# Kernel tuning notes

Hardware: AMD Instinct MI355X
Metric: run time of the kernel (lower is better)

The kernel has to match this reference:

```python
import jax, jax.numpy as jnp
import numpy as np

N_NODES = 50000
N_EDGES = 800000
D_FEAT = 256      # node feature dim F
D_HID = 512       # MLP hidden; MLP input is 2*F = 512
D_OUT = 256


def setup_inputs() -> dict:
    key = jax.random.key(0)
    k = jax.random.split(key, 6)
    x = jax.random.normal(k[0], (N_NODES, D_FEAT), dtype=jnp.float32)
    edge_index = jax.random.randint(k[1], (2, N_EDGES), 0, N_NODES, dtype=jnp.int64)
    # Glorot-ish scaled params for the MLP h_Theta: Linear(2F->H) -> ReLU -> Linear(H->O)
    W1 = jax.random.normal(k[2], (2 * D_FEAT, D_HID), dtype=jnp.float32) / np.sqrt(2 * D_FEAT)
    b1 = jnp.zeros((D_HID,), dtype=jnp.float32)
    W2 = jax.random.normal(k[3], (D_HID, D_OUT), dtype=jnp.float32) / np.sqrt(D_HID)
    b2 = jnp.zeros((D_OUT,), dtype=jnp.float32)
    return {"x": x, "edge_index": edge_index, "W1": W1, "b1": b1, "W2": W2, "b2": b2}


def reference(x, edge_index, W1, b1, W2, b2):
    # EdgeConv: x'_i = sum_{j in N(i)} h_Theta([x_i || x_j - x_i])
    row, col = edge_index[0], edge_index[1]
    xi = x[row]                                   # [E, F] gather (center node)
    feat = jnp.concatenate([xi, x[col] - xi], axis=1)  # [E, 2F]
    h = jax.nn.relu(feat @ W1 + b1)               # [E, H]
    out_e = h @ W2 + b2                           # [E, O]
    # scatter-add back to center nodes (aggr='add')
    return jax.ops.segment_sum(out_e, row, num_segments=x.shape[0])  # [N, O]
```

## Files before the change

### kernel.cpp

```cpp
#include <hip/hip_runtime.h>


#define N_NODES 50000
#define N_EDGES 800000

typedef __attribute__((ext_vector_type(8))) short  bf16x8;
typedef __attribute__((ext_vector_type(8))) unsigned short ushort8;
typedef __attribute__((ext_vector_type(4))) float  f32x4;

#define WCAT_OFF 0u
#define AB_OFF   1048576u
#define W2TH_OFF 205848576u
#define W2TL_OFF 206110720u
#define HIST_OFF 206372864u
#define RS_OFF   206572864u
#define CUR_OFF  206772880u
#define SROW_OFF 206972880u
#define SCOL_OFF 210172880u

__device__ __forceinline__ unsigned short f2bf(float f) {
    unsigned u = __builtin_bit_cast(unsigned, f);
    unsigned r = (u + 0x7fffu + ((u >> 16) & 1u)) >> 16;
    return (unsigned short)r;
}
__device__ __forceinline__ float bf2f(unsigned short h) {
    unsigned u = ((unsigned)h) << 16;
    return __builtin_bit_cast(float, u);
}

__global__ void build_wcat(const float* __restrict__ W1, float* __restrict__ Wcat) {
    int idx = blockIdx.x * 256 + threadIdx.x;
    int k = idx >> 10;
    int c = idx & 1023;
    float v;
    if (c < 512) v = W1[k * 512 + c] - W1[(k + 256) * 512 + c];
    else         v = W1[(k + 256) * 512 + (c - 512)];
    Wcat[idx] = v;
}

__global__ void build_w2t(const float* __restrict__ W2,
                          unsigned short* __restrict__ w2th,
                          unsigned short* __restrict__ w2tl) {
    int idx = blockIdx.x * 256 + threadIdx.x;
    int k = idx >> 8;
    int c = idx & 255;
    float v = W2[idx];
    unsigned short hi = f2bf(v);
    unsigned short lo = f2bf(v - bf2f(hi));
    w2th[c * 512 + k] = hi;
    w2tl[c * 512 + k] = lo;
}

__global__ void zero_out(float4* __restrict__ out) {
    out[(size_t)blockIdx.x * 256 + threadIdx.x] = float4{0.f, 0.f, 0.f, 0.f};
}
__global__ void zero_ints(int* __restrict__ p, int n) {
    int i = blockIdx.x * 256 + threadIdx.x;
    if (i < n) p[i] = 0;
}

__global__ void hist_rows(const int* __restrict__ eidx, int* __restrict__ hist) {
    int e = blockIdx.x * 256 + threadIdx.x;
    if (e < N_EDGES) atomicAdd(&hist[eidx[e]], 1);
}

__global__ void scan50k(const int* __restrict__ hist, int* __restrict__ rowStart,
                        int* __restrict__ cursor) {
    __shared__ int part[1024];
    int t = threadIdx.x;
    int base = t * 49;
    int sum = 0;
    for (int i = 0; i < 49; ++i) {
        int idx = base + i;
        if (idx < N_NODES) sum += hist[idx];
    }
    part[t] = sum;
    __syncthreads();
    for (int off = 1; off < 1024; off <<= 1) {
        int v = (t >= off) ? part[t - off] : 0;
        __syncthreads();
        part[t] += v;
        __syncthreads();
    }
    int run = part[t] - sum;
    for (int i = 0; i < 49; ++i) {
        int idx = base + i;
        if (idx < N_NODES) {
            rowStart[idx] = run;
            cursor[idx]   = run;
            run += hist[idx];
        }
    }
    if (t == 1023) rowStart[N_NODES] = run;
}

__global__ void scatter_edges(const int* __restrict__ eidx, int* __restrict__ cursor,
                              int* __restrict__ srow, int* __restrict__ scol) {
    int e = blockIdx.x * 256 + threadIdx.x;
    if (e >= N_EDGES) return;
    int r = eidx[e];
    int p = atomicAdd(&cursor[r], 1);
    srow[p] = r;
    scol[p] = eidx[N_EDGES + e];
}

__launch_bounds__(256, 2)
__global__ void node_gemm(const float* __restrict__ x, const float* __restrict__ Wcat,
                          const float* __restrict__ b1, float* __restrict__ AB) {
    __shared__ float xT[32][128];
    __shared__ float wT[32][128];
    const int t  = threadIdx.x;
    const int m0 = blockIdx.x * 128;
    const int c0 = blockIdx.y * 128;
    const int er = t >> 4, ec = t & 15;

    float acc[8][8];
    #pragma unroll
    for (int i = 0; i < 8; ++i)
        #pragma unroll
        for (int j = 0; j < 8; ++j) acc[i][j] = 0.f;

    for (int k0 = 0; k0 < 256; k0 += 32) {
        {
            int mr = t & 127, half = t >> 7;
            int row = m0 + mr; if (row >= N_NODES) row = N_NODES - 1;
            const float* src = x + (size_t)row * 256 + k0 + half * 16;
            #pragma unroll
            for (int j = 0; j < 4; ++j) {
                float4 v = *(const float4*)(src + 4 * j);
                int kk = half * 16 + 4 * j;
                xT[kk + 0][mr] = v.x; xT[kk + 1][mr] = v.y;
                xT[kk + 2][mr] = v.z; xT[kk + 3][mr] = v.w;
            }
        }
        {
            int kk = t >> 5, cc = (t & 31) * 4;
            #pragma unroll
            for (int r = 0; r < 4; ++r) {
                float4 v = *(const float4*)(Wcat + (size_t)(k0 + kk + 8 * r) * 1024 + c0 + cc);
                *(float4*)&wT[kk + 8 * r][cc] = v;
            }
        }
        __syncthreads();
        #pragma unroll 4
        for (int kk = 0; kk < 32; ++kk) {
            float a[8], b[8];
            *(float4*)&a[0] = *(const float4*)&xT[kk][er * 8];
            *(float4*)&a[4] = *(const float4*)&xT[kk][er * 8 + 4];
            *(float4*)&b[0] = *(const float4*)&wT[kk][ec * 8];
            *(float4*)&b[4] = *(const float4*)&wT[kk][ec * 8 + 4];
            #pragma unroll
            for (int i = 0; i < 8; ++i)
                #pragma unroll
                for (int j = 0; j < 8; ++j) acc[i][j] += a[i] * b[j];
        }
        __syncthreads();
    }
    float bias[8];
    if (c0 < 512) {
        *(float4*)&bias[0] = *(const float4*)(b1 + c0 + ec * 8);
        *(float4*)&bias[4] = *(const float4*)(b1 + c0 + ec * 8 + 4);
    } else {
        #pragma unroll
        for (int j = 0; j < 8; ++j) bias[j] = 0.f;
    }
    #pragma unroll
    for (int i = 0; i < 8; ++i) {
        int row = m0 + er * 8 + i;
        if (row < N_NODES) {
            float o[8];
            #pragma unroll
            for (int j = 0; j < 8; ++j) o[j] = acc[i][j] + bias[j];
            float* dst = AB + (size_t)row * 1024 + c0 + ec * 8;
            *(float4*)(dst)     = *(float4*)&o[0];
            *(float4*)(dst + 4) = *(float4*)&o[4];
        }
    }
}

__launch_bounds__(256, 2)
__global__ void edge_gemm_mfma(const float* __restrict__ AB,
                               const unsigned short* __restrict__ w2th,
                               const unsigned short* __restrict__ w2tl,
                               const float* __restrict__ b2,
                               const int* __restrict__ srow,
                               const int* __restrict__ scol,
                               float* __restrict__ out) {
    __shared__ unsigned short hHi[2][128][40];
    __shared__ unsigned short hLo[2][128][40];
    __shared__ int rowS[128];

    const int t   = threadIdx.x;
    const int l   = t & 63;
    const int w   = t >> 6;
    const int wc0 = w * 64;
    const int e0  = blockIdx.x * 128;
    const int el  = t & 127;
    const int half = t >> 7;

    if (t < 128) rowS[t] = srow[e0 + t];
    const int rA = srow[e0 + el];
    const int cA = scol[e0 + el];
    const float* rowPtr = AB + (size_t)rA * 1024;
    const float* colPtr = AB + (size_t)cA * 1024 + 512;

    f32x4 acc[8][4];
    #pragma unroll
    for (int i = 0; i < 8; ++i)
        #pragma unroll
        for (int j = 0; j < 4; ++j) acc[i][j] = f32x4{0.f, 0.f, 0.f, 0.f};

    {
        float hv[16];
        #pragma unroll
        for (int q = 0; q < 4; ++q) {
            float4 va = *(const float4*)(rowPtr + half * 16 + 4 * q);
            float4 vb = *(const float4*)(colPtr + half * 16 + 4 * q);
            hv[4 * q + 0] = fmaxf(va.x + vb.x, 0.f);
            hv[4 * q + 1] = fmaxf(va.y + vb.y, 0.f);
            hv[4 * q + 2] = fmaxf(va.z + vb.z, 0.f);
            hv[4 * q + 3] = fmaxf(va.w + vb.w, 0.f);
        }
        unsigned short hs[16], ls[16];
        #pragma unroll
        for (int m = 0; m < 16; ++m) {
            hs[m] = f2bf(hv[m]);
            ls[m] = f2bf(hv[m] - bf2f(hs[m]));
        }
        #pragma unroll
        for (int s = 0; s < 2; ++s) {
            *(ushort8*)(&hHi[0][el][(half * 2 + s) * 8]) = *(ushort8*)&hs[8 * s];
            *(ushort8*)(&hLo[0][el][(half * 2 + s) * 8]) = *(ushort8*)&ls[8 * s];
        }
    }
    __syncthreads();

    const int aoff = (l & 15) * 40 + (l >> 4) * 8;
    const int boff = (wc0 + (l & 15)) * 512 + (l >> 4) * 8;

    for (int step = 0; step < 16; ++step) {
        const int cur = step & 1;
        float4 nA[4], nB[4];
        if (step < 15) {
            const int k0n = (step + 1) * 32 + half * 16;
            #pragma unroll
            for (int q = 0; q < 4; ++q) {
                nA[q] = *(const float4*)(rowPtr + k0n + 4 * q);
                nB[q] = *(const float4*)(colPtr + k0n + 4 * q);
            }
        }
        const int k0 = step * 32;
        bf16x8 bh[4], bl[4];
        #pragma unroll
        for (int j = 0; j < 4; ++j) {
            bh[j] = *(const bf16x8*)(w2th + boff + j * 16 * 512 + k0);
            bl[j] = *(const bf16x8*)(w2tl + boff + j * 16 * 512 + k0);
        }
        const unsigned short* hbH = &hHi[cur][0][0];
        const unsigned short* hbL = &hLo[cur][0][0];
        #pragma unroll
        for (int i = 0; i < 8; ++i) {
            bf16x8 ah = *(const bf16x8*)(hbH + i * 640 + aoff);
            bf16x8 al = *(const bf16x8*)(hbL + i * 640 + aoff);
            #pragma unroll
            for (int j = 0; j < 4; ++j) {
                acc[i][j] = __builtin_amdgcn_mfma_f32_16x16x32_bf16(ah, bh[j], acc[i][j], 0, 0, 0);
                acc[i][j] = __builtin_amdgcn_mfma_f32_16x16x32_bf16(al, bh[j], acc[i][j], 0, 0, 0);
                acc[i][j] = __builtin_amdgcn_mfma_f32_16x16x32_bf16(ah, bl[j], acc[i][j], 0, 0, 0);
            }
        }
        if (step < 15) {
            float hv[16];
            #pragma unroll
            for (int q = 0; q < 4; ++q) {
                hv[4 * q + 0] = fmaxf(nA[q].x + nB[q].x, 0.f);
                hv[4 * q + 1] = fmaxf(nA[q].y + nB[q].y, 0.f);
                hv[4 * q + 2] = fmaxf(nA[q].z + nB[q].z, 0.f);
                hv[4 * q + 3] = fmaxf(nA[q].w + nB[q].w, 0.f);
            }
            unsigned short hs[16], ls[16];
            #pragma unroll
            for (int m = 0; m < 16; ++m) {
                hs[m] = f2bf(hv[m]);
                ls[m] = f2bf(hv[m] - bf2f(hs[m]));
            }
            const int nxt = cur ^ 1;
            #pragma unroll
            for (int s = 0; s < 2; ++s) {
                *(ushort8*)(&hHi[nxt][el][(half * 2 + s) * 8]) = *(ushort8*)&hs[8 * s];
                *(ushort8*)(&hLo[nxt][el][(half * 2 + s) * 8]) = *(ushort8*)&ls[8 * s];
            }
        }
        __syncthreads();
    }

    float bv[4];
    #pragma unroll
    for (int j = 0; j < 4; ++j) bv[j] = b2[wc0 + j * 16 + (l & 15)];
    const int eg = (l >> 4) * 4;
    #pragma unroll
    for (int i = 0; i < 8; ++i) {
        const int eb = i * 16 + eg;
        const int r0 = rowS[eb], r1 = rowS[eb + 1], r2 = rowS[eb + 2], r3 = rowS[eb + 3];
        const bool same = (r0 == r1) & (r1 == r2) & (r2 == r3);
        #pragma unroll
        for (int j = 0; j < 4; ++j) {
            const int col = wc0 + j * 16 + (l & 15);
            f32x4 a = acc[i][j];
            if (same) {
                unsafeAtomicAdd(out + (size_t)r0 * 256 + col,
                                a[0] + a[1] + a[2] + a[3] + 4.f * bv[j]);
            } else {
                unsafeAtomicAdd(out + (size_t)r0 * 256 + col, a[0] + bv[j]);
                unsafeAtomicAdd(out + (size_t)r1 * 256 + col, a[1] + bv[j]);
                unsafeAtomicAdd(out + (size_t)r2 * 256 + col, a[2] + bv[j]);
                unsafeAtomicAdd(out + (size_t)r3 * 256 + col, a[3] + bv[j]);
            }
        }
    }
}

extern "C" void kernel_launch(void* const* d_in, const int* in_sizes, int n_in,
                              void* d_out, int out_size, void* d_ws, size_t ws_size,
                              hipStream_t stream) {
    const float* x   = (const float*)d_in[0];
    const int*   eix = (const int*)d_in[1];
    const float* W1  = (const float*)d_in[2];
    const float* b1  = (const float*)d_in[3];
    const float* W2  = (const float*)d_in[4];
    const float* b2  = (const float*)d_in[5];
    float* out = (float*)d_out;
    char*  ws  = (char*)d_ws;

    float*          Wcat   = (float*)(ws + WCAT_OFF);
    float*          AB     = (float*)(ws + AB_OFF);
    unsigned short* w2th   = (unsigned short*)(ws + W2TH_OFF);
    unsigned short* w2tl   = (unsigned short*)(ws + W2TL_OFF);
    int*            hist   = (int*)(ws + HIST_OFF);
    int*            rowSt  = (int*)(ws + RS_OFF);
    int*            cursor = (int*)(ws + CUR_OFF);
    int*            srow   = (int*)(ws + SROW_OFF);
    int*            scol   = (int*)(ws + SCOL_OFF);

    build_wcat<<<1024, 256, 0, stream>>>(W1, Wcat);
    build_w2t<<<512, 256, 0, stream>>>(W2, w2th, w2tl);
    zero_ints<<<196, 256, 0, stream>>>(hist, N_NODES);
    zero_out<<<12500, 256, 0, stream>>>((float4*)out);
    node_gemm<<<dim3(391, 8), 256, 0, stream>>>(x, Wcat, b1, AB);
    hist_rows<<<3125, 256, 0, stream>>>(eix, hist);
    scan50k<<<1, 1024, 0, stream>>>(hist, rowSt, cursor);
    scatter_edges<<<3125, 256, 0, stream>>>(eix, cursor, srow, scol);
    edge_gemm_mfma<<<6250, 256, 0, stream>>>(AB, w2th, w2tl, b2, srow, scol, out);
}
```

Baseline: 1.623 ms.

## Drop hidden-activation low bf16 split and halve edge tile to 64

The edge GEMM no longer keeps a low-order bf16 residual for the ReLU hidden activations. It now issues two MFMAs per tile instead of three, still splitting W2 into high and low parts. The per-block edge tile drops from 128 to 64 with a 4-thread-per-edge load mapping, which halves the accumulators and LDS and raises the launch bound to 4 blocks per SIMD. The intent is less MFMA work and higher occupancy, at the cost of reduced precision in the hidden activations and more W2 reloads per edge.

New measurement: 1.842 ms. +13.4%, slower.

```diff
diff --git a/kernel.cpp b/kernel.cpp
--- a/kernel.cpp
+++ b/kernel.cpp
@@ -178,7 +178,7 @@
     }
 }
 
-__launch_bounds__(256, 2)
+__launch_bounds__(256, 4)
 __global__ void edge_gemm_mfma(const float* __restrict__ AB,
                                const unsigned short* __restrict__ w2th,
                                const unsigned short* __restrict__ w2tl,
@@ -186,110 +186,87 @@
                                const int* __restrict__ srow,
                                const int* __restrict__ scol,
                                float* __restrict__ out) {
-    __shared__ unsigned short hHi[2][128][40];
-    __shared__ unsigned short hLo[2][128][40];
-    __shared__ int rowS[128];
+    __shared__ unsigned short hHi[2][64][40];
+    __shared__ int rowS[64];
 
     const int t   = threadIdx.x;
     const int l   = t & 63;
     const int w   = t >> 6;
     const int wc0 = w * 64;
-    const int e0  = blockIdx.x * 128;
-    const int el  = t & 127;
-    const int half = t >> 7;
-
-    if (t < 128) rowS[t] = srow[e0 + t];
+    const int e0  = blockIdx.x * 64;
+    const int el  = t >> 2;
+    const int q   = t & 3;
+
+    if (t < 64) rowS[t] = srow[e0 + t];
     const int rA = srow[e0 + el];
     const int cA = scol[e0 + el];
     const float* rowPtr = AB + (size_t)rA * 1024;
     const float* colPtr = AB + (size_t)cA * 1024 + 512;
 
-    f32x4 acc[8][4];
-    #pragma unroll
-    for (int i = 0; i < 8; ++i)
+    f32x4 acc[4][4];
+    #pragma unroll
+    for (int i = 0; i < 4; ++i)
         #pragma unroll
         for (int j = 0; j < 4; ++j) acc[i][j] = f32x4{0.f, 0.f, 0.f, 0.f};
 
     {
-        float hv[16];
-        #pragma unroll
-        for (int q = 0; q < 4; ++q) {
-            float4 va = *(const float4*)(rowPtr + half * 16 + 4 * q);
-            float4 vb = *(const float4*)(colPtr + half * 16 + 4 * q);
-            hv[4 * q + 0] = fmaxf(va.x + vb.x, 0.f);
-            hv[4 * q + 1] = fmaxf(va.y + vb.y, 0.f);
-            hv[4 * q + 2] = fmaxf(va.z + vb.z, 0.f);
-            hv[4 * q + 3] = fmaxf(va.w + vb.w, 0.f);
-        }
-        unsigned short hs[16], ls[16];
-        #pragma unroll
-        for (int m = 0; m < 16; ++m) {
-            hs[m] = f2bf(hv[m]);
-            ls[m] = f2bf(hv[m] - bf2f(hs[m]));
-        }
-        #pragma unroll
-        for (int s = 0; s < 2; ++s) {
-            *(ushort8*)(&hHi[0][el][(half * 2 + s) * 8]) = *(ushort8*)&hs[8 * s];
-            *(ushort8*)(&hLo[0][el][(half * 2 + s) * 8]) = *(ushort8*)&ls[8 * s];
-        }
+        float4 a0 = *(const float4*)(rowPtr + q * 8);
+        float4 a1 = *(const float4*)(rowPtr + q * 8 + 4);
+        float4 b0 = *(const float4*)(colPtr + q * 8);
+        float4 b1 = *(const float4*)(colPtr + q * 8 + 4);
+        unsigned short hs[8];
+        hs[0] = f2bf(fmaxf(a0.x + b0.x, 0.f));
+        hs[1] = f2bf(fmaxf(a0.y + b0.y, 0.f));
+        hs[2] = f2bf(fmaxf(a0.z + b0.z, 0.f));
+        hs[3] = f2bf(fmaxf(a0.w + b0.w, 0.f));
+        hs[4] = f2bf(fmaxf(a1.x + b1.x, 0.f));
+        hs[5] = f2bf(fmaxf(a1.y + b1.y, 0.f));
+        hs[6] = f2bf(fmaxf(a1.z + b1.z, 0.f));
+        hs[7] = f2bf(fmaxf(a1.w + b1.w, 0.f));
+        *(ushort8*)(&hHi[0][el][q * 8]) = *(ushort8*)&hs[0];
     }
     __syncthreads();
 
-    const int aoff = (l & 15) * 40 + (l >> 4) * 8;
     const int boff = (wc0 + (l & 15)) * 512 + (l >> 4) * 8;
+    const int arow = l & 15;
+    const int aslot = (l >> 4) * 8;
 
     for (int step = 0; step < 16; ++step) {
         const int cur = step & 1;
-        float4 nA[4], nB[4];
+        float4 nA0, nA1, nB0, nB1;
         if (step < 15) {
-            const int k0n = (step + 1) * 32 + half * 16;
-            #pragma unroll
-            for (int q = 0; q < 4; ++q) {
-                nA[q] = *(const float4*)(rowPtr + k0n + 4 * q);
-                nB[q] = *(const float4*)(colPtr + k0n + 4 * q);
+            const int k0n = (step + 1) * 32 + q * 8;
+            nA0 = *(const float4*)(rowPtr + k0n);
+            nA1 = *(const float4*)(rowPtr + k0n + 4);
+            nB0 = *(const float4*)(colPtr + k0n);
+            nB1 = *(const float4*)(colPtr + k0n + 4);
+        }
+        bf16x8 ah[4];
+        #pragma unroll
+        for (int i = 0; i < 4; ++i)
+            ah[i] = *(const bf16x8*)(&hHi[cur][i * 16 + arow][aslot]);
+        const int k0 = step * 32;
+        #pragma unroll
+        for (int j = 0; j < 4; ++j) {
+            bf16x8 bh = *(const bf16x8*)(w2th + boff + j * 16 * 512 + k0);
+            bf16x8 bl = *(const bf16x8*)(w2tl + boff + j * 16 * 512 + k0);
+            #pragma unroll
+            for (int i = 0; i < 4; ++i) {
+                acc[i][j] = __builtin_amdgcn_mfma_f32_16x16x32_bf16(ah[i], bh, acc[i][j], 0, 0, 0);
+                acc[i][j] = __builtin_amdgcn_mfma_f32_16x16x32_bf16(ah[i], bl, acc[i][j], 0, 0, 0);
             }
         }
-        const int k0 = step * 32;
-        bf16x8 bh[4], bl[4];
-        #pragma unroll
-        for (int j = 0; j < 4; ++j) {
-            bh[j] = *(const bf16x8*)(w2th + boff + j * 16 * 512 + k0);
-            bl[j] = *(const bf16x8*)(w2tl + boff + j * 16 * 512 + k0);
-        }
-        const unsigned short* hbH = &hHi[cur][0][0];
-        const unsigned short* hbL = &hLo[cur][0][0];
-        #pragma unroll
-        for (int i = 0; i < 8; ++i) {
-            bf16x8 ah = *(const bf16x8*)(hbH + i * 640 + aoff);
-            bf16x8 al = *(const bf16x8*)(hbL + i * 640 + aoff);
-            #pragma unroll
-            for (int j = 0; j < 4; ++j) {
-                acc[i][j] = __builtin_amdgcn_mfma_f32_16x16x32_bf16(ah, bh[j], acc[i][j], 0, 0, 0);
-                acc[i][j] = __builtin_amdgcn_mfma_f32_16x16x32_bf16(al, bh[j], acc[i][j], 0, 0, 0);
-                acc[i][j] = __builtin_amdgcn_mfma_f32_16x16x32_bf16(ah, bl[j], acc[i][j], 0, 0, 0);
-            }
-        }
         if (step < 15) {
-            float hv[16];
-            #pragma unroll
-            for (int q = 0; q < 4; ++q) {
-                hv[4 * q + 0] = fmaxf(nA[q].x + nB[q].x, 0.f);
-                hv[4 * q + 1] = fmaxf(nA[q].y + nB[q].y, 0.f);
-                hv[4 * q + 2] = fmaxf(nA[q].z + nB[q].z, 0.f);
-                hv[4 * q + 3] = fmaxf(nA[q].w + nB[q].w, 0.f);
-            }
-            unsigned short hs[16], ls[16];
-            #pragma unroll
-            for (int m = 0; m < 16; ++m) {
-                hs[m] = f2bf(hv[m]);
-                ls[m] = f2bf(hv[m] - bf2f(hs[m]));
-            }
-            const int nxt = cur ^ 1;
-            #pragma unroll
-            for (int s = 0; s < 2; ++s) {
-                *(ushort8*)(&hHi[nxt][el][(half * 2 + s) * 8]) = *(ushort8*)&hs[8 * s];
-                *(ushort8*)(&hLo[nxt][el][(half * 2 + s) * 8]) = *(ushort8*)&ls[8 * s];
-            }
+            unsigned short hs[8];
+            hs[0] = f2bf(fmaxf(nA0.x + nB0.x, 0.f));
+            hs[1] = f2bf(fmaxf(nA0.y + nB0.y, 0.f));
+            hs[2] = f2bf(fmaxf(nA0.z + nB0.z, 0.f));
+            hs[3] = f2bf(fmaxf(nA0.w + nB0.w, 0.f));
+            hs[4] = f2bf(fmaxf(nA1.x + nB1.x, 0.f));
+            hs[5] = f2bf(fmaxf(nA1.y + nB1.y, 0.f));
+            hs[6] = f2bf(fmaxf(nA1.z + nB1.z, 0.f));
+            hs[7] = f2bf(fmaxf(nA1.w + nB1.w, 0.f));
+            *(ushort8*)(&hHi[cur ^ 1][el][q * 8]) = *(ushort8*)&hs[0];
         }
         __syncthreads();
     }
@@ -299,7 +276,7 @@
     for (int j = 0; j < 4; ++j) bv[j] = b2[wc0 + j * 16 + (l & 15)];
     const int eg = (l >> 4) * 4;
     #pragma unroll
-    for (int i = 0; i < 8; ++i) {
+    for (int i = 0; i < 4; ++i) {
         const int eb = i * 16 + eg;
         const int r0 = rowS[eb], r1 = rowS[eb + 1], r2 = rowS[eb + 2], r3 = rowS[eb + 3];
         const bool same = (r0 == r1) & (r1 == r2) & (r2 == r3);
@@ -350,5 +327,5 @@
     hist_rows<<<3125, 256, 0, stream>>>(eix, hist);
     scan50k<<<1, 1024, 0, stream>>>(hist, rowSt, cursor);
     scatter_edges<<<3125, 256, 0, stream>>>(eix, cursor, srow, scol);
-    edge_gemm_mfma<<<6250, 256, 0, stream>>>(AB, w2th, w2tl, b2, srow, scol, out);
-}
+    edge_gemm_mfma<<<12500, 256, 0, stream>>>(AB, w2th, w2tl, b2, srow, scol, out);
+}
```
